# Kernel optimization log

Hardware: AMD Instinct MI355X
Metric: run time of the kernel (lower is better)

Reference implementation:

```python
import jax, jax.numpy as jnp
import numpy as np

B, V, S, H = 16384, 16, 64, 512


def setup_inputs() -> dict:
    key = jax.random.key(0)
    kx, kw, kb, kws, kbs = jax.random.split(key, 5)
    x = jax.random.normal(kx, (B, V, S), dtype=jnp.float32)
    # per-variable linear layers: weight [V, S, H], bias [V, H]
    W = jax.random.normal(kw, (V, S, H), dtype=jnp.float32) * (1.0 / np.sqrt(S))
    b = jax.random.normal(kb, (V, H), dtype=jnp.float32) * 0.01
    # variable selection linear: hidden -> V
    W_sel = jax.random.normal(kws, (H, V), dtype=jnp.float32) * (1.0 / np.sqrt(H))
    b_sel = jax.random.normal(kbs, (V,), dtype=jnp.float32) * 0.01
    return {"x": x, "W": W, "b": b, "W_sel": W_sel, "b_sel": b_sel}


def reference(x, W, b, W_sel, b_sel):
    # per-variable linears: [B, V, H]
    transformed = jnp.einsum('bvs,vsh->bvh', x, W) + b  # grouped small GEMMs
    # torch stacks to [B, H, V]; mean over variable axis -> [B, H]
    flat = transformed.mean(axis=1)
    # softmax-gated selection weights [B, V] (dropout is identity in eval)
    weights = jax.nn.softmax(flat @ W_sel + b_sel, axis=-1)
    # weighted sum over variables -> [B, H]
    out = jnp.einsum('bvh,bv->bh', transformed, weights)
    return out
```

## Files before the change

kernel.cpp:

```cpp
#include <hip/hip_runtime.h>
#include <hip/hip_bf16.h>
#include <stdint.h>

#define B_ROWS 16384
#define VDIM   16
#define SDIM   64
#define HDIM   512
#define KDIM   1024
#define KP2    1088

#define ASTR     1064
#define G_PLOG   68096
#define G_WLDS   (68096 + 8704)
#define G_LDS    (68096 + 8704 + 2048)

using bf16x8 = __attribute__((ext_vector_type(8))) __bf16;
using u16x8  = __attribute__((ext_vector_type(8))) unsigned short;
using f32x4  = __attribute__((ext_vector_type(4))) float;

__device__ __forceinline__ unsigned short f2bf(float f) {
  unsigned int u = __builtin_bit_cast(unsigned int, f);
  u = (u + 0x7FFFu + ((u >> 16) & 1u)) >> 16;
  return (unsigned short)u;
}
__device__ __forceinline__ float bf2f(unsigned short s) {
  return __builtin_bit_cast(float, (unsigned int)s << 16);
}

__device__ __forceinline__ void gl_lds16(const void* g, void* l) {
  __builtin_amdgcn_global_load_lds(
      (const __attribute__((address_space(1))) unsigned int*)(uintptr_t)g,
      (__attribute__((address_space(3))) unsigned int*)(unsigned int)(uintptr_t)l,
      16, 0, 0);
}

__global__ __launch_bounds__(256) void k0_prep(
    const float* __restrict__ W, const float* __restrict__ bias,
    const float* __restrict__ Wsel, const float* __restrict__ bsel,
    unsigned short* __restrict__ Bt, unsigned short* __restrict__ WcombT,
    float* __restrict__ bcomb) {
  __shared__ float bm[HDIM];
  __shared__ float part[16][17];
  __shared__ unsigned short tile[32][264];
  const int t = threadIdx.x;
  if (blockIdx.x < 68) {
    const int k0 = (blockIdx.x >> 1) * 32;
    const int n  = ((blockIdx.x & 1) << 8) + t;
    #pragma unroll 8
    for (int kk = 0; kk < 32; ++kk) {
      const int k = k0 + kk;
      float val;
      if (k < KDIM)            val = W[(size_t)k * HDIM + n];
      else if (k < KDIM + 16)  val = bias[(size_t)(k - KDIM) * HDIM + n];
      else                     val = 0.f;
      tile[kk][t] = f2bf(val);
    }
    __syncthreads();
    unsigned short* dst = Bt + (size_t)n * KP2 + k0;
    #pragma unroll
    for (int seg = 0; seg < 4; ++seg) {
      unsigned short o[8];
      #pragma unroll
      for (int jj = 0; jj < 8; ++jj) o[jj] = tile[seg * 8 + jj][t];
      *(u16x8*)(dst + seg * 8) = *(const u16x8*)o;
    }
    return;
  }
  const int bid = blockIdx.x - 68;
  if (bid < 256) {
    const int wave = t >> 6, lane = t & 63;
    const int k = bid * 4 + wave;
    const float* wr = W + (size_t)k * HDIM;
    float s[16];
    #pragma unroll
    for (int v = 0; v < 16; ++v) s[v] = 0.f;
    #pragma unroll
    for (int j = 0; j < 8; ++j) {
      const int h = lane + 64 * j;
      const float a = wr[h];
      const float4* wl = (const float4*)(Wsel + h * 16);
      const float4 q0 = wl[0], q1 = wl[1], q2 = wl[2], q3 = wl[3];
      s[0]  = fmaf(a, q0.x, s[0]);  s[1]  = fmaf(a, q0.y, s[1]);
      s[2]  = fmaf(a, q0.z, s[2]);  s[3]  = fmaf(a, q0.w, s[3]);
      s[4]  = fmaf(a, q1.x, s[4]);  s[5]  = fmaf(a, q1.y, s[5]);
      s[6]  = fmaf(a, q1.z, s[6]);  s[7]  = fmaf(a, q1.w, s[7]);
      s[8]  = fmaf(a, q2.x, s[8]);  s[9]  = fmaf(a, q2.y, s[9]);
      s[10] = fmaf(a, q2.z, s[10]); s[11] = fmaf(a, q2.w, s[11]);
      s[12] = fmaf(a, q3.x, s[12]); s[13] = fmaf(a, q3.y, s[13]);
      s[14] = fmaf(a, q3.z, s[14]); s[15] = fmaf(a, q3.w, s[15]);
    }
    #pragma unroll
    for (int off = 32; off > 0; off >>= 1) {
      #pragma unroll
      for (int v = 0; v < 16; ++v) s[v] += __shfl_xor(s[v], off, 64);
    }
    float mine = 0.f;
    #pragma unroll
    for (int v = 0; v < 16; ++v) mine = (lane == v) ? s[v] : mine;
    if (lane < 16) WcombT[lane * KDIM + k] = f2bf(mine * (1.f / 16.f));
  } else {
    for (int h = t; h < HDIM; h += 256) {
      float s = 0.f;
      #pragma unroll
      for (int v = 0; v < VDIM; ++v) s += bias[v * HDIM + h];
      bm[h] = s * (1.f / 16.f);
    }
    __syncthreads();
    int v = t & 15, sl = t >> 4;
    float s = 0.f;
    for (int h = sl * 32; h < sl * 32 + 32; ++h) s = fmaf(bm[h], Wsel[h * VDIM + v], s);
    part[sl][v] = s;
    __syncthreads();
    if (t < 16) {
      float s2 = bsel[t];
      #pragma unroll
      for (int i = 0; i < 16; ++i) s2 += part[i][t];
      bcomb[t] = s2;
    }
  }
}

__global__ __launch_bounds__(512, 4) void k1_gate(
    const float* __restrict__ x, const unsigned short* __restrict__ WcombT,
    const float* __restrict__ bcomb, unsigned short* __restrict__ Ap,
    int rowbase) {
  extern __shared__ unsigned short As[];
  float* plog = (float*)((char*)As + G_PLOG);
  float* wlds = (float*)((char*)As + G_WLDS);

  const int t = threadIdx.x;
  const int lrow0 = blockIdx.x * 32;
  const int grow0 = rowbase + lrow0;
  const int wave = t >> 6, lane = t & 63;
  const int mlane = lane & 15, quad = lane >> 4;
  const int srow = t >> 4;
  const int sc = (t & 15) * 8;

  u16x8 xreg[8];
  {
    const float* xr = x + (size_t)(grow0 + srow) * KDIM + sc;
    unsigned short* aw = As + srow * ASTR + sc;
    #pragma unroll
    for (int i = 0; i < 8; ++i) {
      const f32x4 a0 = __builtin_nontemporal_load((const f32x4*)(xr + i * 128));
      const f32x4 a1 = __builtin_nontemporal_load((const f32x4*)(xr + i * 128 + 4));
      u16x8 u;
      u[0] = f2bf(a0[0]); u[1] = f2bf(a0[1]); u[2] = f2bf(a0[2]); u[3] = f2bf(a0[3]);
      u[4] = f2bf(a1[0]); u[5] = f2bf(a1[1]); u[6] = f2bf(a1[2]); u[7] = f2bf(a1[3]);
      xreg[i] = u;
      *(u16x8*)(aw + i * 128) = u;
    }
  }
  __syncthreads();

  {
    const int kh = wave >> 1, rg = wave & 1;
    const unsigned short* al = As + (rg * 16 + mlane) * ASTR + kh * 256 + quad * 8;
    const unsigned short* bl = WcombT + mlane * KDIM + kh * 256 + quad * 8;
    f32x4 acc = {0.f, 0.f, 0.f, 0.f};
    #pragma unroll
    for (int kt = 0; kt < 8; ++kt) {
      bf16x8 a = *(const bf16x8*)al; al += 32;
      bf16x8 b = *(const bf16x8*)bl; bl += 32;
      acc = __builtin_amdgcn_mfma_f32_16x16x32_bf16(a, b, acc, 0, 0, 0);
    }
    float* pl = plog + ((size_t)((kh * 2 + rg) * 16 + quad * 4) * 17 + mlane);
    #pragma unroll
    for (int r = 0; r < 4; ++r) pl[r * 17] = acc[r];
  }
  __syncthreads();

  if (t < 32) {
    const int rg = t >> 4, rr = t & 15;
    float l[16];
    float mx = -1e30f;
    #pragma unroll
    for (int v = 0; v < 16; ++v) {
      float s = bcomb[v];
      #pragma unroll
      for (int kq = 0; kq < 4; ++kq)
        s += plog[((size_t)((kq * 2 + rg) * 16 + rr)) * 17 + v];
      l[v] = s;
      mx = fmaxf(mx, s);
    }
    float s = 0.f;
    #pragma unroll
    for (int v = 0; v < 16; ++v) { l[v] = __expf(l[v] - mx); s += l[v]; }
    const float inv = 1.f / s;
    float* wo = wlds + t * 16;
    #pragma unroll
    for (int v = 0; v < 16; ++v) wo[v] = l[v] * inv;
  }
  __syncthreads();

  {
    float wv[16];
    const f32x4* wq = (const f32x4*)(wlds + srow * 16);
    #pragma unroll
    for (int q = 0; q < 4; ++q) {
      const f32x4 f = wq[q];
      wv[4 * q + 0] = f[0]; wv[4 * q + 1] = f[1];
      wv[4 * q + 2] = f[2]; wv[4 * q + 3] = f[3];
    }
    const int vbase = (t & 15) >> 3;
    unsigned short* aw = Ap + (size_t)(lrow0 + srow) * KP2 + sc;
    #pragma unroll
    for (int i = 0; i < 8; ++i) {
      const float w = wv[2 * i + vbase];
      const u16x8 a = xreg[i];
      u16x8 o;
      #pragma unroll
      for (int j = 0; j < 8; ++j) o[j] = f2bf(w * bf2f(a[j]));
      *(u16x8*)(aw + i * 128) = o;
    }
    const int seg = t & 15;
    if (seg < 8) {
      u16x8 o;
      #pragma unroll
      for (int jj = 0; jj < 8; ++jj) {
        const int c = seg * 8 + jj;
        o[jj] = (c < 16) ? f2bf(wv[c]) : (unsigned short)0;
      }
      *(u16x8*)(Ap + (size_t)(lrow0 + srow) * KP2 + KDIM + seg * 8) = o;
    }
  }
}

__global__ __launch_bounds__(256) void k2_gemm(
    const unsigned short* __restrict__ Ap, const unsigned short* __restrict__ Bt,
    float* __restrict__ C, int rowbase) {
  __shared__ unsigned short As[8192];
  __shared__ unsigned short Bs[8192];

  const int t = threadIdx.x;
  const int nwg = gridDim.x;
  const int q = nwg >> 3, r = nwg & 7;
  const int xcd = blockIdx.x & 7, idx = blockIdx.x >> 3;
  const int bid = (xcd < r ? xcd * (q + 1) : r * (q + 1) + (xcd - r) * q) + idx;

  const int lrowb = (bid >> 2) * 128;
  const int colb  = (bid & 3) * 128;
  const int wave = t >> 6, lane = t & 63;
  const int mlane = lane & 15, quad = lane >> 4;
  const int wr = wave >> 1, wc = wave & 1;

  const int l8 = lane >> 3, lk = (lane & 7) * 8;
  const unsigned short* asrc[4];
  const unsigned short* bsrc[4];
  #pragma unroll
  for (int i = 0; i < 4; ++i) {
    asrc[i] = Ap + (size_t)(lrowb + wave * 32 + i * 8 + l8) * KP2 + lk;
    bsrc[i] = Bt + (size_t)(colb + wave * 32 + i * 8 + l8) * KP2 + lk;
  }
  unsigned short* adst = As + wave * 2048;
  unsigned short* bdst = Bs + wave * 2048;

  f32x4 acc[4][4];
  const f32x4 z = {0.f, 0.f, 0.f, 0.f};
  #pragma unroll
  for (int i = 0; i < 4; ++i)
    #pragma unroll
    for (int j = 0; j < 4; ++j) acc[i][j] = z;

  #pragma unroll 1
  for (int kt = 0; kt < 17; ++kt) {
    #pragma unroll
    for (int i = 0; i < 4; ++i) gl_lds16(asrc[i], adst + i * 512);
    #pragma unroll
    for (int i = 0; i < 4; ++i) gl_lds16(bsrc[i], bdst + i * 512);
    #pragma unroll
    for (int i = 0; i < 4; ++i) { asrc[i] += 64; bsrc[i] += 64; }
    __syncthreads();

    #pragma unroll
    for (int ks = 0; ks < 2; ++ks) {
      bf16x8 av[4], bv[4];
      #pragma unroll
      for (int i = 0; i < 4; ++i)
        av[i] = *(const bf16x8*)(As + (wr * 64 + i * 16 + mlane) * 64 + ks * 32 + quad * 8);
      #pragma unroll
      for (int j = 0; j < 4; ++j)
        bv[j] = *(const bf16x8*)(Bs + (wc * 64 + j * 16 + mlane) * 64 + ks * 32 + quad * 8);
      #pragma unroll
      for (int i = 0; i < 4; ++i)
        #pragma unroll
        for (int j = 0; j < 4; ++j)
          acc[i][j] = __builtin_amdgcn_mfma_f32_16x16x32_bf16(av[i], bv[j], acc[i][j], 0, 0, 0);
    }
    __syncthreads();
  }

  #pragma unroll
  for (int i = 0; i < 4; ++i)
    #pragma unroll
    for (int j = 0; j < 4; ++j)
      #pragma unroll
      for (int r2 = 0; r2 < 4; ++r2) {
        const size_t row = (size_t)rowbase + lrowb + wr * 64 + i * 16 + quad * 4 + r2;
        const int col = colb + wc * 64 + j * 16 + mlane;
        __builtin_nontemporal_store(acc[i][j][r2], &C[row * HDIM + col]);
      }
}

extern "C" void kernel_launch(void* const* d_in, const int* in_sizes, int n_in,
                              void* d_out, int out_size, void* d_ws, size_t ws_size,
                              hipStream_t stream) {
  const float* x    = (const float*)d_in[0];
  const float* W    = (const float*)d_in[1];
  const float* bias = (const float*)d_in[2];
  const float* Wsel = (const float*)d_in[3];
  const float* bsel = (const float*)d_in[4];
  float* out = (float*)d_out;

  char* ws = (char*)d_ws;
  unsigned short* Bt     = (unsigned short*)(ws);
  unsigned short* WcombT = (unsigned short*)(ws + 1114112);
  float*          bcomb  = (float*)(ws + 1146880);
  unsigned short* Ap     = (unsigned short*)(ws + 1147136);

  const size_t fixed = 1147136;
  size_t avail = (ws_size > fixed) ? (ws_size - fixed) : 0;
  size_t maxRows = avail / (KP2 * 2);
  int sliceRows = (int)((maxRows / 128) * 128);
  if (sliceRows > B_ROWS) sliceRows = B_ROWS;
  if (sliceRows < 128) sliceRows = 128;

  static int lds_set = 0;
  if (!lds_set) {
    hipFuncSetAttribute((const void*)k1_gate,
                        hipFuncAttributeMaxDynamicSharedMemorySize, G_LDS);
    lds_set = 1;
  }

  k0_prep<<<325, 256, 0, stream>>>(W, bias, Wsel, bsel, Bt, WcombT, bcomb);
  for (int r0 = 0; r0 < B_ROWS; r0 += sliceRows) {
    const int rows = (B_ROWS - r0 < sliceRows) ? (B_ROWS - r0) : sliceRows;
    k1_gate<<<rows / 32, 512, G_LDS, stream>>>(x, WcombT, bcomb, Ap, r0);
    k2_gemm<<<(rows / 128) * 4, 256, 0, stream>>>(Ap, Bt, out, r0);
  }
}
```

Measured before the change: 165.5 us.

## Double-buffer LDS tiles in k2_gemm to overlap global loads with MFMA

Splits the shared-memory A and B tiles into two buffers and prefetches the next K-tile through direct global-to-LDS loads while MFMAs run on the current tile. The per-iteration pair of __syncthreads becomes one explicit vmcnt wait plus barrier, with sched_barriers pinning the instruction order. This aims to hide global load latency behind compute, at the cost of doubling LDS use to 64KB per block, which may lower occupancy.

```diff
diff --git a/kernel.cpp b/kernel.cpp
--- a/kernel.cpp
+++ b/kernel.cpp
@@ -8,6 +8,7 @@
 #define HDIM   512
 #define KDIM   1024
 #define KP2    1088
+#define BK     64
 
 #define ASTR     1064
 #define G_PLOG   68096
@@ -229,8 +230,8 @@
 __global__ __launch_bounds__(256) void k2_gemm(
     const unsigned short* __restrict__ Ap, const unsigned short* __restrict__ Bt,
     float* __restrict__ C, int rowbase) {
-  __shared__ unsigned short As[8192];
-  __shared__ unsigned short Bs[8192];
+  __shared__ unsigned short As[2][128 * BK];
+  __shared__ unsigned short Bs[2][128 * BK];
 
   const int t = threadIdx.x;
   const int nwg = gridDim.x;
@@ -252,8 +253,17 @@
     asrc[i] = Ap + (size_t)(lrowb + wave * 32 + i * 8 + l8) * KP2 + lk;
     bsrc[i] = Bt + (size_t)(colb + wave * 32 + i * 8 + l8) * KP2 + lk;
   }
-  unsigned short* adst = As + wave * 2048;
-  unsigned short* bdst = Bs + wave * 2048;
+  const int ldst = (wave * 32) * BK;
+
+  #pragma unroll
+  for (int i = 0; i < 4; ++i) gl_lds16(asrc[i], &As[0][ldst + i * 8 * BK]);
+  #pragma unroll
+  for (int i = 0; i < 4; ++i) gl_lds16(bsrc[i], &Bs[0][ldst + i * 8 * BK]);
+  #pragma unroll
+  for (int i = 0; i < 4; ++i) { asrc[i] += BK; bsrc[i] += BK; }
+  asm volatile("s_waitcnt vmcnt(0)" ::: "memory");
+  __builtin_amdgcn_s_barrier();
+  __builtin_amdgcn_sched_barrier(0);
 
   f32x4 acc[4][4];
   const f32x4 z = {0.f, 0.f, 0.f, 0.f};
@@ -264,30 +274,34 @@
 
   #pragma unroll 1
   for (int kt = 0; kt < 17; ++kt) {
-    #pragma unroll
-    for (int i = 0; i < 4; ++i) gl_lds16(asrc[i], adst + i * 512);
-    #pragma unroll
-    for (int i = 0; i < 4; ++i) gl_lds16(bsrc[i], bdst + i * 512);
-    #pragma unroll
-    for (int i = 0; i < 4; ++i) { asrc[i] += 64; bsrc[i] += 64; }
-    __syncthreads();
-
+    const int cur = kt & 1;
+    if (kt < 16) {
+      #pragma unroll
+      for (int i = 0; i < 4; ++i) gl_lds16(asrc[i], &As[cur ^ 1][ldst + i * 8 * BK]);
+      #pragma unroll
+      for (int i = 0; i < 4; ++i) gl_lds16(bsrc[i], &Bs[cur ^ 1][ldst + i * 8 * BK]);
+      #pragma unroll
+      for (int i = 0; i < 4; ++i) { asrc[i] += BK; bsrc[i] += BK; }
+    }
     #pragma unroll
     for (int ks = 0; ks < 2; ++ks) {
       bf16x8 av[4], bv[4];
       #pragma unroll
       for (int i = 0; i < 4; ++i)
-        av[i] = *(const bf16x8*)(As + (wr * 64 + i * 16 + mlane) * 64 + ks * 32 + quad * 8);
+        av[i] = *(const bf16x8*)(&As[cur][(wr * 64 + i * 16 + mlane) * BK + ks * 32 + quad * 8]);
       #pragma unroll
       for (int j = 0; j < 4; ++j)
-        bv[j] = *(const bf16x8*)(Bs + (wc * 64 + j * 16 + mlane) * 64 + ks * 32 + quad * 8);
+        bv[j] = *(const bf16x8*)(&Bs[cur][(wc * 64 + j * 16 + mlane) * BK + ks * 32 + quad * 8]);
       #pragma unroll
       for (int i = 0; i < 4; ++i)
         #pragma unroll
         for (int j = 0; j < 4; ++j)
           acc[i][j] = __builtin_amdgcn_mfma_f32_16x16x32_bf16(av[i], bv[j], acc[i][j], 0, 0, 0);
     }
-    __syncthreads();
+    __builtin_amdgcn_sched_barrier(0);
+    asm volatile("s_waitcnt vmcnt(0)" ::: "memory");
+    __builtin_amdgcn_s_barrier();
+    __builtin_amdgcn_sched_barrier(0);
   }
 
   #pragma unroll
```

Result: faster. 161.6 us (-2.4%).
